# Kernel tuning notes

Measured on AMD Instinct MI355X. Metric: run time of the kernel, lower is better.

Reference implementation:

```python
import jax, jax.numpy as jnp
import numpy as np

NEG = 9e15

def adj_helper(adj):
    n = adj.shape[0]
    a = adj + jnp.eye(n, dtype=adj.dtype)
    d1 = jnp.sqrt(a.sum(axis=-1))[:, None]
    d2 = jnp.sqrt(a.sum(axis=0))[None, :]
    return a / d1 / d2

def gcn(adj, x, Ws):
    a = adj_helper(adj)
    z = x
    for W in Ws:
        z = jax.nn.elu(a @ (z @ W))
    return z

def sage(adj, x, layers):
    deg = jnp.clip(adj.sum(axis=-1, keepdims=True), 1e-5, None)
    a = adj / deg
    z = x
    for (Wp, b, W) in layers:
        h = jax.nn.elu(z @ Wp + b)
        h = a @ h
        z = jax.nn.elu(jnp.concatenate([z, h], axis=1) @ W)
    return z

def sim_graph_cos(h, k):
    n = h.shape[0]
    length = jnp.sqrt(jnp.sum(h * h, axis=-1))          # [n]
    sim = (h @ h.T) / (length[:, None] * length[None, :])
    sim = sim - jnp.eye(n, dtype=sim.dtype) * NEG        # mask self
    val, ids = jax.lax.top_k(sim, k)                     # [n,k]
    rows = jnp.arange(n)[:, None]
    return jnp.zeros_like(sim).at[rows, ids].set(val)

def setup_inputs() -> dict:
    key = jax.random.key(0)
    ks = jax.random.split(key, 16)
    N, F, H, E, K = 6144, 128, 128, 16384, 32
    s = 0.05
    adj = (jax.random.uniform(ks[0], (N, N)) < 0.002).astype(jnp.float32)
    x = jax.random.normal(ks[1], (N, F), dtype=jnp.float32)
    src = jax.random.randint(ks[2], (E,), 0, N)
    dst = jax.random.randint(ks[3], (E,), 0, N)
    labels = (jax.random.uniform(ks[4], (E,)) < 0.5).astype(jnp.float32)
    return {
        "src": src, "dst": dst, "labels": labels, "adj": adj, "x": x,
        "Wg1": jax.random.normal(ks[5], (F, H)) * s,
        "Wg2": jax.random.normal(ks[6], (H, H)) * s,
        "Wp1": jax.random.normal(ks[7], (F, H)) * s,
        "b1": jax.random.normal(ks[8], (1, H)) * s,
        "Ws1": jax.random.normal(ks[9], (F + H, H)) * s,
        "Wp2": jax.random.normal(ks[10], (H, H)) * s,
        "b2": jax.random.normal(ks[11], (1, H)) * s,
        "Ws2": jax.random.normal(ks[12], (H + H, H)) * s,
        "PredW": jax.random.normal(ks[13], (2 * H, 2 * H)) * s,
        "PredB": jax.random.normal(ks[14], (1, 1)) * s,
        "top_k": 32,
    }

def reference(src, dst, labels, adj, x, Wg1, Wg2, Wp1, b1, Ws1, Wp2, b2, Ws2, PredW, PredB, top_k):
    h1 = gcn(adj, x, [Wg1, Wg2])                 # [N,H]
    sim_adj = sim_graph_cos(x, top_k)            # [N,N] top-k sparse (dense-stored)
    h2 = sage(sim_adj, x, [(Wp1, b1, Ws1), (Wp2, b2, Ws2)])  # [N,H]
    h = jnp.concatenate([h1, h2], axis=1)        # [N,2H]
    src_h = h[src]                               # [E,2H]
    dst_h = h[dst]                               # [E,2H]
    logits = jnp.einsum('ed,df,ef->e', src_h, PredW, dst_h) + PredB[0, 0]
    # BCEWithLogitsLoss (mean, numerically stable)
    loss = jnp.mean(jnp.maximum(logits, 0) - logits * labels
                    + jnp.log1p(jnp.exp(-jnp.abs(logits))))
    return loss, logits
```

## Files before the change

kernel.cpp:

```cpp
#include <hip/hip_runtime.h>
#include <hip/hip_bf16.h>
#include <stdint.h>

#define N_NODES 6144
#define FDIM    128
#define EEDGES  16384
#define KTOP    32
#define KSEL    48
#define MAXNBR  64
#define MAXCAND 512
#define NTILES  96
#define GRIDY   16
#define TPB     (NTILES/GRIDY)

typedef short bf16x8 __attribute__((ext_vector_type(8)));
typedef float f32x4  __attribute__((ext_vector_type(4)));

__device__ __forceinline__ float elu_f(float x){ return x > 0.f ? x : expm1f(x); }

__device__ __forceinline__ unsigned short f2bf(float f){
  unsigned int u = __float_as_uint(f);
  u += 0x7FFFu + ((u >> 16) & 1u);
  return (unsigned short)(u >> 16);
}
__device__ __forceinline__ float bf2f(unsigned short h){
  return __uint_as_float(((unsigned int)h) << 16);
}

__global__ __launch_bounds__(256) void prep(const float* __restrict__ adj,
    const float* __restrict__ x, int* __restrict__ nbr, int* __restrict__ nbrcnt,
    int* __restrict__ colcnt, unsigned short* __restrict__ xbf,
    float* __restrict__ xninv, float* __restrict__ cat1){
  const int b = blockIdx.x, t = threadIdx.x;
  if (b < N_NODES){
    const int i = b;
    __shared__ int s_cnt;
    if (t == 0) s_cnt = 0;
    __syncthreads();
    const float4* row = (const float4*)(adj + (size_t)i * N_NODES);
    for (int v = t; v < N_NODES/4; v += 256){
      float4 f = row[v];
      int c = v * 4;
      if (f.x != 0.f){ int s = atomicAdd(&s_cnt,1); if (s < MAXNBR) nbr[i*MAXNBR+s] = c;   atomicAdd(&colcnt[c],1); }
      if (f.y != 0.f){ int s = atomicAdd(&s_cnt,1); if (s < MAXNBR) nbr[i*MAXNBR+s] = c+1; atomicAdd(&colcnt[c+1],1); }
      if (f.z != 0.f){ int s = atomicAdd(&s_cnt,1); if (s < MAXNBR) nbr[i*MAXNBR+s] = c+2; atomicAdd(&colcnt[c+2],1); }
      if (f.w != 0.f){ int s = atomicAdd(&s_cnt,1); if (s < MAXNBR) nbr[i*MAXNBR+s] = c+3; atomicAdd(&colcnt[c+3],1); }
    }
    __syncthreads();
    if (t == 0) nbrcnt[i] = min(s_cnt, MAXNBR);
  } else {
    const int i = (b - N_NODES)*2 + (t >> 7);
    const int tl = t & 127;
    float v = x[(size_t)i*FDIM + tl];
    xbf[(size_t)i*FDIM + tl] = f2bf(v);
    cat1[(size_t)i*256 + tl] = v;
    float s = v * v;
    for (int o = 32; o > 0; o >>= 1) s += __shfl_down(s, o, 64);
    __shared__ float ws[4];
    if ((t & 63) == 0) ws[t >> 6] = s;
    __syncthreads();
    if (tl == 0) xninv[i] = rsqrtf(ws[(t>>7)*2] + ws[(t>>7)*2 + 1]);
  }
}

__global__ __launch_bounds__(256) void simgemm(const unsigned short* __restrict__ xbf,
    const float* __restrict__ xninv, unsigned short* __restrict__ sim,
    float* __restrict__ gmax){
  const int t    = threadIdx.x;
  const int R0   = blockIdx.x * 32;
  const int tb0  = blockIdx.y * TPB;
  const int lane = t & 63, w = t >> 6;
  const int lr   = lane & 15, q8 = (lane >> 4) * 8, quad = lane >> 4;

  __shared__ unsigned short Abf[32][136];
  __shared__ unsigned short Bbf[64][136];
  __shared__ unsigned short Stile[32][72];
  __shared__ float nrow[32];
  __shared__ float ncol[64];
  __shared__ float wmax[4][32];

  for (int e = t; e < 32*16; e += 256){
    int r = e >> 4, c8 = e & 15;
    *(uint4*)&Abf[r][c8*8] = ((const uint4*)(xbf + (size_t)(R0 + r)*FDIM))[c8];
  }
  if (t < 32) nrow[t] = xninv[R0 + t];

  for (int tb = tb0; tb < tb0 + TPB; ++tb){
    __syncthreads();
    for (int e = t; e < 64*16; e += 256){
      int r = e >> 4, c8 = e & 15;
      *(uint4*)&Bbf[r][c8*8] = ((const uint4*)(xbf + (size_t)(tb*64 + r)*FDIM))[c8];
    }
    if (t < 64) ncol[t] = xninv[tb*64 + t];
    __syncthreads();

    f32x4 acc[2] = {};
#pragma unroll
    for (int kb = 0; kb < 4; ++kb){
      bf16x8 bcol  = *(const bf16x8*)&Bbf[w*16 + lr][kb*32 + q8];
      bf16x8 arow0 = *(const bf16x8*)&Abf[lr      ][kb*32 + q8];
      bf16x8 arow1 = *(const bf16x8*)&Abf[16 + lr ][kb*32 + q8];
      acc[0] = __builtin_amdgcn_mfma_f32_16x16x32_bf16(bcol, arow0, acc[0], 0, 0, 0);
      acc[1] = __builtin_amdgcn_mfma_f32_16x16x32_bf16(bcol, arow1, acc[1], 0, 0, 0);
    }
    const int scol0 = w*16 + quad*4;
    const float nc0 = ncol[scol0], nc1 = ncol[scol0+1],
                nc2 = ncol[scol0+2], nc3 = ncol[scol0+3];
#pragma unroll
    for (int f = 0; f < 2; ++f){
      const int srow = f*16 + lr;
      const float nr = nrow[srow];
      const int grow = R0 + srow, gcol0 = tb*64 + scol0;
      float v0 = acc[f][0]*nr*nc0, v1 = acc[f][1]*nr*nc1,
            v2 = acc[f][2]*nr*nc2, v3 = acc[f][3]*nr*nc3;
      if (grow == gcol0    ) v0 = -2.0f;
      if (grow == gcol0 + 1) v1 = -2.0f;
      if (grow == gcol0 + 2) v2 = -2.0f;
      if (grow == gcol0 + 3) v3 = -2.0f;
      unsigned int h0 = f2bf(v0), h1 = f2bf(v1), h2 = f2bf(v2), h3 = f2bf(v3);
      uint2 p; p.x = h0 | (h1 << 16); p.y = h2 | (h3 << 16);
      *(uint2*)&Stile[srow][scol0] = p;
      float rmax = fmaxf(fmaxf(bf2f(h0), bf2f(h1)), fmaxf(bf2f(h2), bf2f(h3)));
      rmax = fmaxf(rmax, __shfl_xor(rmax, 16, 64));
      rmax = fmaxf(rmax, __shfl_xor(rmax, 32, 64));
      if (quad == 0) wmax[w][srow] = rmax;
    }
    __syncthreads();
    {
      int r = t >> 3, c8 = t & 7;
      *(uint4*)&sim[(size_t)(R0 + r)*N_NODES + tb*64 + c8*8] = *(uint4*)&Stile[r][c8*8];
    }
    if (t < 32){
      float g = fmaxf(fmaxf(wmax[0][t], wmax[1][t]), fmaxf(wmax[2][t], wmax[3][t]));
      gmax[(size_t)(R0 + t)*NTILES + tb] = g;
    }
  }
}

__global__ __launch_bounds__(256) void refine_scan(const float* __restrict__ x,
    const float* __restrict__ xninv, const unsigned short* __restrict__ sim,
    const float* __restrict__ gmax, float* __restrict__ tval, int* __restrict__ tidx,
    float* __restrict__ deginv){
  const int i = blockIdx.x, t = threadIdx.x;
  __shared__ float xi[128];
  __shared__ float gm[NTILES];
  __shared__ float tauv;
  __shared__ float cv[MAXCAND];
  __shared__ int   ci[MAXCAND];
  __shared__ float sel[KTOP];
  __shared__ int   cnt;
  if (t == 0) cnt = 0;
  if (t < 32) *(float4*)&xi[t*4] = *(const float4*)(x + (size_t)i*FDIM + t*4);
  if (t < NTILES) gm[t] = gmax[(size_t)i*NTILES + t];
  __syncthreads();
  if (t < NTILES){
    float v = gm[t]; int rank = 0;
    for (int j = 0; j < NTILES; ++j){
      float u = gm[j];
      if (u > v || (u == v && j < t)) rank++;
    }
    if (rank == KSEL-1) tauv = v;
  }
  __syncthreads();
  const float taui = tauv;
  const uint4* srow = (const uint4*)(sim + (size_t)i*N_NODES);
  for (int v8 = t; v8 < N_NODES/8; v8 += 256){
    uint4 u = srow[v8];
    const unsigned short* h = (const unsigned short*)&u;
#pragma unroll
    for (int q = 0; q < 8; ++q){
      if (bf2f(h[q]) >= taui){
        int s = atomicAdd(&cnt, 1);
        if (s < MAXCAND) ci[s] = v8*8 + q;
      }
    }
  }
  __syncthreads();
  int n = cnt; if (n > MAXCAND) n = MAXCAND;
  const float ni = xninv[i];
  const int part = t & 3, cb = t >> 2;
  for (int c0 = 0; c0 < n; c0 += 64){
    const int c = c0 + cb;
    float acc = 0.f;
    int idx = 0;
    if (c < n){
      idx = ci[c];
      const float* xc = x + (size_t)idx*FDIM + part*32;
#pragma unroll
      for (int q = 0; q < 8; ++q){
        float4 f = *(const float4*)(xc + q*4);
        const float* a = &xi[part*32 + q*4];
        acc += a[0]*f.x + a[1]*f.y + a[2]*f.z + a[3]*f.w;
      }
    }
    acc += __shfl_xor(acc, 1, 64);
    acc += __shfl_xor(acc, 2, 64);
    if (c < n && part == 0) cv[c] = acc * ni * xninv[idx];
  }
  __syncthreads();
  for (int c = t; c < n; c += 256){
    float v = cv[c]; int id = ci[c];
    int rank = 0;
    for (int j = 0; j < n; ++j){
      float u = cv[j];
      if (u > v || (u == v && ci[j] < id)) rank++;
    }
    if (rank < KTOP){
      tval[(size_t)i*KTOP + rank] = v;
      tidx[(size_t)i*KTOP + rank] = id;
      sel[rank] = v;
    }
  }
  __syncthreads();
  if (t == 0){
    float s = 0.f;
    for (int q = 0; q < KTOP; ++q) s += sel[q];
    deginv[i] = 1.0f / fmaxf(s, 1e-5f);
  }
}

__global__ __launch_bounds__(256) void gemm_dual(const float* __restrict__ A,
    const float* __restrict__ B1, const float* __restrict__ B2,
    const float* __restrict__ bias2, float* __restrict__ C1, float* __restrict__ C2,
    const int* __restrict__ nbrcnt, const int* __restrict__ colcnt,
    float* __restrict__ d1inv, float* __restrict__ d2inv){
  const int t = threadIdx.x;
  const int R0 = blockIdx.x * 32, C0 = blockIdx.y * 64;
  if (blockIdx.y == 0 && t < 32){
    int i = R0 + t;
    d1inv[i] = rsqrtf((float)(nbrcnt[i] + 1));
    d2inv[i] = rsqrtf((float)(colcnt[i] + 1));
  }
  const int rg = t >> 4, cg = t & 15;
  __shared__ float Alds[32][34];
  __shared__ float B1lds[32][68];
  __shared__ float B2lds[32][68];
  float4 p0 = {0,0,0,0}, p1 = {0,0,0,0};
  float4 q0 = {0,0,0,0}, q1 = {0,0,0,0};
  for (int kc = 0; kc < FDIM; kc += 32){
    __syncthreads();
    { int r = t >> 3, k0 = (t & 7) * 4;
      float4 f = *(const float4*)(A + (size_t)(R0 + r)*FDIM + kc + k0);
      Alds[k0+0][r] = f.x; Alds[k0+1][r] = f.y; Alds[k0+2][r] = f.z; Alds[k0+3][r] = f.w; }
#pragma unroll
    for (int e = 0; e < 2; ++e){
      int idx = t + e*256;
      int k = idx >> 4, m4 = idx & 15;
      *(float4*)&B1lds[k][m4*4] = *(const float4*)(B1 + (size_t)(kc + k)*FDIM + C0 + m4*4);
      *(float4*)&B2lds[k][m4*4] = *(const float4*)(B2 + (size_t)(kc + k)*FDIM + C0 + m4*4);
    }
    __syncthreads();
#pragma unroll
    for (int k = 0; k < 32; ++k){
      float2 a = *(const float2*)&Alds[k][rg*2];
      float4 b = *(const float4*)&B1lds[k][cg*4];
      float4 c = *(const float4*)&B2lds[k][cg*4];
      p0.x += a.x*b.x; p0.y += a.x*b.y; p0.z += a.x*b.z; p0.w += a.x*b.w;
      p1.x += a.y*b.x; p1.y += a.y*b.y; p1.z += a.y*b.z; p1.w += a.y*b.w;
      q0.x += a.x*c.x; q0.y += a.x*c.y; q0.z += a.x*c.z; q0.w += a.x*c.w;
      q1.x += a.y*c.x; q1.y += a.y*c.y; q1.z += a.y*c.z; q1.w += a.y*c.w;
    }
  }
  const int r0 = R0 + rg*2, c0 = C0 + cg*4;
  *(float4*)&C1[(size_t)r0*FDIM + c0] = p0;
  *(float4*)&C1[(size_t)(r0+1)*FDIM + c0] = p1;
  float4 bb = *(const float4*)&bias2[c0];
  q0.x = elu_f(q0.x + bb.x); q0.y = elu_f(q0.y + bb.y); q0.z = elu_f(q0.z + bb.z); q0.w = elu_f(q0.w + bb.w);
  q1.x = elu_f(q1.x + bb.x); q1.y = elu_f(q1.y + bb.y); q1.z = elu_f(q1.z + bb.z); q1.w = elu_f(q1.w + bb.w);
  *(float4*)&C2[(size_t)r0*FDIM + c0] = q0;
  *(float4*)&C2[(size_t)(r0+1)*FDIM + c0] = q1;
}

template<int M>
__global__ __launch_bounds__(256) void gemm_k(const float* __restrict__ A, int lda,
    const float* __restrict__ B, const float* __restrict__ bias,
    float* __restrict__ C, int ldc, int K, int act){
  const int t = threadIdx.x;
  const int R0 = blockIdx.x * 32, C0 = blockIdx.y * 64;
  const int rg = t >> 4, cg = t & 15;
  __shared__ float Alds[32][34];
  __shared__ float Blds[32][68];
  float4 acc0 = {0,0,0,0}, acc1 = {0,0,0,0};
  for (int kc = 0; kc < K; kc += 32){
    __syncthreads();
    { int r = t >> 3, k0 = (t & 7) * 4;
      float4 f = *(const float4*)(A + (size_t)(R0 + r)*lda + kc + k0);
      Alds[k0+0][r] = f.x; Alds[k0+1][r] = f.y; Alds[k0+2][r] = f.z; Alds[k0+3][r] = f.w; }
#pragma unroll
    for (int e = 0; e < 2; ++e){
      int idx = t + e*256;
      int k = idx >> 4, m4 = idx & 15;
      *(float4*)&Blds[k][m4*4] = *(const float4*)(B + (size_t)(kc + k)*M + C0 + m4*4);
    }
    __syncthreads();
#pragma unroll
    for (int k = 0; k < 32; ++k){
      float2 a = *(const float2*)&Alds[k][rg*2];
      float4 b = *(const float4*)&Blds[k][cg*4];
      acc0.x += a.x*b.x; acc0.y += a.x*b.y; acc0.z += a.x*b.z; acc0.w += a.x*b.w;
      acc1.x += a.y*b.x; acc1.y += a.y*b.y; acc1.z += a.y*b.z; acc1.w += a.y*b.w;
    }
  }
  const int r0 = R0 + rg*2, c0 = C0 + cg*4;
  float4 bb = {0,0,0,0};
  if (bias) bb = *(const float4*)&bias[c0];
  acc0.x += bb.x; acc0.y += bb.y; acc0.z += bb.z; acc0.w += bb.w;
  acc1.x += bb.x; acc1.y += bb.y; acc1.z += bb.z; acc1.w += bb.w;
  if (act){
    acc0.x = elu_f(acc0.x); acc0.y = elu_f(acc0.y); acc0.z = elu_f(acc0.z); acc0.w = elu_f(acc0.w);
    acc1.x = elu_f(acc1.x); acc1.y = elu_f(acc1.y); acc1.z = elu_f(acc1.z); acc1.w = elu_f(acc1.w);
  }
  *(float4*)&C[(size_t)r0*ldc + c0] = acc0;
  *(float4*)&C[(size_t)(r0+1)*ldc + c0] = acc1;
}

__global__ __launch_bounds__(128) void spmm_gcn(const float* __restrict__ T,
    const int* __restrict__ nbr, const int* __restrict__ nbrcnt,
    const float* __restrict__ d1inv, const float* __restrict__ d2inv,
    float* __restrict__ C, int ldc){
  const int i = blockIdx.x, t = threadIdx.x;
  float acc = T[(size_t)i*FDIM + t] * d2inv[i];
  const int cnt = nbrcnt[i];
  const int* nb = nbr + (size_t)i*MAXNBR;
  for (int s = 0; s < cnt; ++s){
    int j = nb[s];
    acc += T[(size_t)j*FDIM + t] * d2inv[j];
  }
  C[(size_t)i*ldc + t] = elu_f(acc * d1inv[i]);
}

__global__ __launch_bounds__(128) void spmm_sage(const float* __restrict__ P,
    const float* __restrict__ tval, const int* __restrict__ tidx,
    const float* __restrict__ deginv, float* __restrict__ C, int ldc){
  const int i = blockIdx.x, t = threadIdx.x;
  float acc = 0.f;
  const float* vv = tval + (size_t)i*KTOP;
  const int*   ii = tidx + (size_t)i*KTOP;
  for (int s = 0; s < KTOP; ++s)
    acc += vv[s] * P[(size_t)ii[s]*FDIM + t];
  C[(size_t)i*ldc + t] = acc * deginv[i];
}

__global__ __launch_bounds__(128) void spmm_pair(const float* __restrict__ T1,
    const int* __restrict__ nbr, const int* __restrict__ nbrcnt,
    const float* __restrict__ d1inv, const float* __restrict__ d2inv,
    float* __restrict__ z1,
    const float* __restrict__ T2, const float* __restrict__ tval,
    const int* __restrict__ tidx, const float* __restrict__ deginv,
    float* __restrict__ cat1r){
  const int b = blockIdx.x, t = threadIdx.x;
  if (b < N_NODES){
    const int i = b;
    float acc = T1[(size_t)i*FDIM + t] * d2inv[i];
    const int cnt = nbrcnt[i];
    const int* nb = nbr + (size_t)i*MAXNBR;
    for (int s = 0; s < cnt; ++s){
      int j = nb[s];
      acc += T1[(size_t)j*FDIM + t] * d2inv[j];
    }
    z1[(size_t)i*FDIM + t] = elu_f(acc * d1inv[i]);
  } else {
    const int i = b - N_NODES;
    float acc = 0.f;
    const float* vv = tval + (size_t)i*KTOP;
    const int*   ii = tidx + (size_t)i*KTOP;
    for (int s = 0; s < KTOP; ++s)
      acc += vv[s] * T2[(size_t)ii[s]*FDIM + t];
    cat1r[(size_t)i*256 + t] = acc * deginv[i];
  }
}

__global__ __launch_bounds__(256) void edge_loss(const int* __restrict__ src,
    const int* __restrict__ dst, const float* __restrict__ labels,
    const float* __restrict__ HP, const float* __restrict__ hcat,
    const float* __restrict__ predB, float* __restrict__ out,
    float* __restrict__ partial){
  const int t = threadIdx.x;
  const int e = blockIdx.x*4 + (t >> 6);
  const int lane = t & 63;
  const int s = src[e], d = dst[e];
  const float* hp = HP   + (size_t)s*256;
  const float* hc = hcat + (size_t)d*256;
  float acc = 0.f;
  for (int k = lane; k < 256; k += 64) acc += hp[k] * hc[k];
  for (int o = 32; o > 0; o >>= 1) acc += __shfl_down(acc, o, 64);
  __shared__ float terms[4];
  if (lane == 0){
    float l = acc + predB[0];
    out[1 + e] = l;
    float y = labels[e];
    terms[t >> 6] = fmaxf(l, 0.f) - l*y + log1pf(expf(-fabsf(l)));
  }
  __syncthreads();
  if (t == 0) partial[blockIdx.x] = terms[0] + terms[1] + terms[2] + terms[3];
}

__global__ __launch_bounds__(256) void reduce_loss(const float* __restrict__ partial,
    float* __restrict__ out){
  const int t = threadIdx.x, lane = t & 63, w = t >> 6;
  float s = 0.f;
  for (int i = t; i < EEDGES/4; i += 256) s += partial[i];
  for (int o = 32; o > 0; o >>= 1) s += __shfl_down(s, o, 64);
  __shared__ float ws[4];
  if (lane == 0) ws[w] = s;
  __syncthreads();
  if (t == 0) out[0] = (ws[0] + ws[1] + ws[2] + ws[3]) * (1.0f / EEDGES);
}

extern "C" void kernel_launch(void* const* d_in, const int* in_sizes, int n_in,
                              void* d_out, int out_size, void* d_ws, size_t ws_size,
                              hipStream_t stream){
  (void)in_sizes; (void)n_in; (void)out_size; (void)ws_size;
  const int*   src    = (const int*)d_in[0];
  const int*   dst    = (const int*)d_in[1];
  const float* labels = (const float*)d_in[2];
  const float* adj    = (const float*)d_in[3];
  const float* x      = (const float*)d_in[4];
  const float* Wg1    = (const float*)d_in[5];
  const float* Wg2    = (const float*)d_in[6];
  const float* Wp1    = (const float*)d_in[7];
  const float* b1     = (const float*)d_in[8];
  const float* Ws1    = (const float*)d_in[9];
  const float* Wp2    = (const float*)d_in[10];
  const float* b2     = (const float*)d_in[11];
  const float* Ws2    = (const float*)d_in[12];
  const float* PredW  = (const float*)d_in[13];
  const float* PredB  = (const float*)d_in[14];

  char* ws = (char*)d_ws;
  size_t off = 0;
  auto alloc = [&](size_t bytes)->void*{
    void* p = ws + off; off += (bytes + 255) & ~(size_t)255; return p; };

  int*   colcnt = (int*)  alloc((size_t)N_NODES*4);
  int*   nbrcnt = (int*)  alloc((size_t)N_NODES*4);
  int*   nbr    = (int*)  alloc((size_t)N_NODES*MAXNBR*4);
  float* d1inv  = (float*)alloc((size_t)N_NODES*4);
  float* d2inv  = (float*)alloc((size_t)N_NODES*4);
  float* xninv  = (float*)alloc((size_t)N_NODES*4);
  unsigned short* xbf = (unsigned short*)alloc((size_t)N_NODES*FDIM*2);
  float* tval   = (float*)alloc((size_t)N_NODES*KTOP*4);
  int*   tidx   = (int*)  alloc((size_t)N_NODES*KTOP*4);
  float* dginv  = (float*)alloc((size_t)N_NODES*4);
  float* gmax   = (float*)alloc((size_t)N_NODES*NTILES*4);
  float* partial= (float*)alloc((size_t)(EEDGES/4)*4);
  float* T1     = (float*)alloc((size_t)N_NODES*FDIM*4);
  float* T2     = (float*)alloc((size_t)N_NODES*FDIM*4);
  float* cat1   = (float*)alloc((size_t)N_NODES*256*4);
  float* cat2   = (float*)alloc((size_t)N_NODES*256*4);
  float* hcat   = (float*)alloc((size_t)N_NODES*256*4);
  unsigned short* sim = (unsigned short*)alloc((size_t)N_NODES*N_NODES*2);
  float* z1     = cat2;
  float* out    = (float*)d_out;

  hipMemsetAsync(colcnt, 0, (size_t)N_NODES*4, stream);

  prep       <<<N_NODES + N_NODES/2, 256, 0, stream>>>(adj, x, nbr, nbrcnt, colcnt, xbf, xninv, cat1);
  simgemm    <<<dim3(N_NODES/32, GRIDY), 256, 0, stream>>>(xbf, xninv, sim, gmax);
  refine_scan<<<N_NODES, 256, 0, stream>>>(x, xninv, sim, gmax, tval, tidx, dginv);

  gemm_dual  <<<dim3(N_NODES/32, 2), 256, 0, stream>>>(x, Wg1, Wp1, b1, T1, T2,
                                                       nbrcnt, colcnt, d1inv, d2inv);
  spmm_pair  <<<2*N_NODES, 128, 0, stream>>>(T1, nbr, nbrcnt, d1inv, d2inv, z1,
                                             T2, tval, tidx, dginv, cat1 + 128);

  gemm_k<128><<<dim3(N_NODES/32, 2), 256, 0, stream>>>(z1, FDIM, Wg2, nullptr, T1, FDIM, 128, 0);
  spmm_gcn   <<<N_NODES, 128, 0, stream>>>(T1, nbr, nbrcnt, d1inv, d2inv, hcat, 256);

  gemm_k<128><<<dim3(N_NODES/32, 2), 256, 0, stream>>>(cat1, 256, Ws1, nullptr, cat2, 256, 256, 1);

  gemm_k<128><<<dim3(N_NODES/32, 2), 256, 0, stream>>>(cat2, 256, Wp2, b2, T1, FDIM, 128, 1);
  spmm_sage  <<<N_NODES, 128, 0, stream>>>(T1, tval, tidx, dginv, cat2 + 128, 256);
  gemm_k<128><<<dim3(N_NODES/32, 2), 256, 0, stream>>>(cat2, 256, Ws2, nullptr, hcat + 128, 256, 256, 1);

  gemm_k<256><<<dim3(N_NODES/32, 4), 256, 0, stream>>>(hcat, 256, PredW, nullptr, cat1, 256, 256, 0);
  edge_loss  <<<EEDGES/4, 256, 0, stream>>>(src, dst, labels, cat1, hcat, PredB, out, partial);
  reduce_loss<<<1, 256, 0, stream>>>(partial, out);
}
```

Baseline: 483.8 us.

## Merge independent GCN and SAGE stages into shared launches; enlarge simgemm row tile

Independent GEMMs from the GCN and SAGE branches (Wg2 and Ws1) now run in one launch, and the GCN spmm runs alongside the Wp2 GEMM in a second, with blocks split by index. This cuts kernel launches and lets small, under-filled grids overlap on the GPU. z1 gets its own buffer so it no longer aliases cat2. The similarity GEMM now tiles 64 rows per block instead of 32, reusing each B-tile load across four MFMAs per wave, at the cost of more LDS and a grid half as large.

```diff
diff --git a/kernel.cpp b/kernel.cpp
--- a/kernel.cpp
+++ b/kernel.cpp
@@ -67,23 +67,23 @@
     const float* __restrict__ xninv, unsigned short* __restrict__ sim,
     float* __restrict__ gmax){
   const int t    = threadIdx.x;
-  const int R0   = blockIdx.x * 32;
+  const int R0   = blockIdx.x * 64;
   const int tb0  = blockIdx.y * TPB;
   const int lane = t & 63, w = t >> 6;
   const int lr   = lane & 15, q8 = (lane >> 4) * 8, quad = lane >> 4;
 
-  __shared__ unsigned short Abf[32][136];
+  __shared__ unsigned short Abf[64][136];
   __shared__ unsigned short Bbf[64][136];
-  __shared__ unsigned short Stile[32][72];
-  __shared__ float nrow[32];
+  __shared__ unsigned short Stile[64][72];
+  __shared__ float nrow[64];
   __shared__ float ncol[64];
-  __shared__ float wmax[4][32];
-
-  for (int e = t; e < 32*16; e += 256){
+  __shared__ float wmax[4][64];
+
+  for (int e = t; e < 64*16; e += 256){
     int r = e >> 4, c8 = e & 15;
     *(uint4*)&Abf[r][c8*8] = ((const uint4*)(xbf + (size_t)(R0 + r)*FDIM))[c8];
   }
-  if (t < 32) nrow[t] = xninv[R0 + t];
+  if (t < 64) nrow[t] = xninv[R0 + t];
 
   for (int tb = tb0; tb < tb0 + TPB; ++tb){
     __syncthreads();
@@ -94,20 +94,21 @@
     if (t < 64) ncol[t] = xninv[tb*64 + t];
     __syncthreads();
 
-    f32x4 acc[2] = {};
+    f32x4 acc[4] = {};
 #pragma unroll
     for (int kb = 0; kb < 4; ++kb){
-      bf16x8 bcol  = *(const bf16x8*)&Bbf[w*16 + lr][kb*32 + q8];
-      bf16x8 arow0 = *(const bf16x8*)&Abf[lr      ][kb*32 + q8];
-      bf16x8 arow1 = *(const bf16x8*)&Abf[16 + lr ][kb*32 + q8];
-      acc[0] = __builtin_amdgcn_mfma_f32_16x16x32_bf16(bcol, arow0, acc[0], 0, 0, 0);
-      acc[1] = __builtin_amdgcn_mfma_f32_16x16x32_bf16(bcol, arow1, acc[1], 0, 0, 0);
+      bf16x8 bcol = *(const bf16x8*)&Bbf[w*16 + lr][kb*32 + q8];
+#pragma unroll
+      for (int f = 0; f < 4; ++f){
+        bf16x8 arow = *(const bf16x8*)&Abf[f*16 + lr][kb*32 + q8];
+        acc[f] = __builtin_amdgcn_mfma_f32_16x16x32_bf16(bcol, arow, acc[f], 0, 0, 0);
+      }
     }
     const int scol0 = w*16 + quad*4;
     const float nc0 = ncol[scol0], nc1 = ncol[scol0+1],
                 nc2 = ncol[scol0+2], nc3 = ncol[scol0+3];
 #pragma unroll
-    for (int f = 0; f < 2; ++f){
+    for (int f = 0; f < 4; ++f){
       const int srow = f*16 + lr;
       const float nr = nrow[srow];
       const int grow = R0 + srow, gcol0 = tb*64 + scol0;
@@ -126,11 +127,13 @@
       if (quad == 0) wmax[w][srow] = rmax;
     }
     __syncthreads();
-    {
-      int r = t >> 3, c8 = t & 7;
+#pragma unroll
+    for (int e0 = 0; e0 < 2; ++e0){
+      int e = t + e0*256;
+      int r = e >> 3, c8 = e & 7;
       *(uint4*)&sim[(size_t)(R0 + r)*N_NODES + tb*64 + c8*8] = *(uint4*)&Stile[r][c8*8];
     }
-    if (t < 32){
+    if (t < 64){
       float g = fmaxf(fmaxf(wmax[0][t], wmax[1][t]), fmaxf(wmax[2][t], wmax[3][t]));
       gmax[(size_t)(R0 + t)*NTILES + tb] = g;
     }
@@ -219,6 +222,47 @@
   }
 }
 
+__device__ __forceinline__ void gemm_body(const float* __restrict__ A, int lda,
+    const float* __restrict__ B, int ldb, const float* __restrict__ bias,
+    float* __restrict__ C, int ldc, int K, int act, int R0, int C0){
+  const int t = threadIdx.x;
+  const int rg = t >> 4, cg = t & 15;
+  __shared__ float Alds[32][34];
+  __shared__ float Blds[32][68];
+  float4 acc0 = {0,0,0,0}, acc1 = {0,0,0,0};
+  for (int kc = 0; kc < K; kc += 32){
+    __syncthreads();
+    { int r = t >> 3, k0 = (t & 7) * 4;
+      float4 f = *(const float4*)(A + (size_t)(R0 + r)*lda + kc + k0);
+      Alds[k0+0][r] = f.x; Alds[k0+1][r] = f.y; Alds[k0+2][r] = f.z; Alds[k0+3][r] = f.w; }
+#pragma unroll
+    for (int e = 0; e < 2; ++e){
+      int idx = t + e*256;
+      int k = idx >> 4, m4 = idx & 15;
+      *(float4*)&Blds[k][m4*4] = *(const float4*)(B + (size_t)(kc + k)*ldb + C0 + m4*4);
+    }
+    __syncthreads();
+#pragma unroll
+    for (int k = 0; k < 32; ++k){
+      float2 a = *(const float2*)&Alds[k][rg*2];
+      float4 b = *(const float4*)&Blds[k][cg*4];
+      acc0.x += a.x*b.x; acc0.y += a.x*b.y; acc0.z += a.x*b.z; acc0.w += a.x*b.w;
+      acc1.x += a.y*b.x; acc1.y += a.y*b.y; acc1.z += a.y*b.z; acc1.w += a.y*b.w;
+    }
+  }
+  const int r0 = R0 + rg*2, c0 = C0 + cg*4;
+  float4 bb = {0,0,0,0};
+  if (bias) bb = *(const float4*)&bias[c0];
+  acc0.x += bb.x; acc0.y += bb.y; acc0.z += bb.z; acc0.w += bb.w;
+  acc1.x += bb.x; acc1.y += bb.y; acc1.z += bb.z; acc1.w += bb.w;
+  if (act){
+    acc0.x = elu_f(acc0.x); acc0.y = elu_f(acc0.y); acc0.z = elu_f(acc0.z); acc0.w = elu_f(acc0.w);
+    acc1.x = elu_f(acc1.x); acc1.y = elu_f(acc1.y); acc1.z = elu_f(acc1.z); acc1.w = elu_f(acc1.w);
+  }
+  *(float4*)&C[(size_t)r0*ldc + c0] = acc0;
+  *(float4*)&C[(size_t)(r0+1)*ldc + c0] = acc1;
+}
+
 __global__ __launch_bounds__(256) void gemm_dual(const float* __restrict__ A,
     const float* __restrict__ B1, const float* __restrict__ B2,
     const float* __restrict__ bias2, float* __restrict__ C1, float* __restrict__ C2,
@@ -275,70 +319,7 @@
 __global__ __launch_bounds__(256) void gemm_k(const float* __restrict__ A, int lda,
     const float* __restrict__ B, const float* __restrict__ bias,
     float* __restrict__ C, int ldc, int K, int act){
-  const int t = threadIdx.x;
-  const int R0 = blockIdx.x * 32, C0 = blockIdx.y * 64;
-  const int rg = t >> 4, cg = t & 15;
-  __shared__ float Alds[32][34];
-  __shared__ float Blds[32][68];
-  float4 acc0 = {0,0,0,0}, acc1 = {0,0,0,0};
-  for (int kc = 0; kc < K; kc += 32){
-    __syncthreads();
-    { int r = t >> 3, k0 = (t & 7) * 4;
-      float4 f = *(const float4*)(A + (size_t)(R0 + r)*lda + kc + k0);
-      Alds[k0+0][r] = f.x; Alds[k0+1][r] = f.y; Alds[k0+2][r] = f.z; Alds[k0+3][r] = f.w; }
-#pragma unroll
-    for (int e = 0; e < 2; ++e){
-      int idx = t + e*256;
-      int k = idx >> 4, m4 = idx & 15;
-      *(float4*)&Blds[k][m4*4] = *(const float4*)(B + (size_t)(kc + k)*M + C0 + m4*4);
-    }
-    __syncthreads();
-#pragma unroll
-    for (int k = 0; k < 32; ++k){
-      float2 a = *(const float2*)&Alds[k][rg*2];
-      float4 b = *(const float4*)&Blds[k][cg*4];
-      acc0.x += a.x*b.x; acc0.y += a.x*b.y; acc0.z += a.x*b.z; acc0.w += a.x*b.w;
-      acc1.x += a.y*b.x; acc1.y += a.y*b.y; acc1.z += a.y*b.z; acc1.w += a.y*b.w;
-    }
-  }
-  const int r0 = R0 + rg*2, c0 = C0 + cg*4;
-  float4 bb = {0,0,0,0};
-  if (bias) bb = *(const float4*)&bias[c0];
-  acc0.x += bb.x; acc0.y += bb.y; acc0.z += bb.z; acc0.w += bb.w;
-  acc1.x += bb.x; acc1.y += bb.y; acc1.z += bb.z; acc1.w += bb.w;
-  if (act){
-    acc0.x = elu_f(acc0.x); acc0.y = elu_f(acc0.y); acc0.z = elu_f(acc0.z); acc0.w = elu_f(acc0.w);
-    acc1.x = elu_f(acc1.x); acc1.y = elu_f(acc1.y); acc1.z = elu_f(acc1.z); acc1.w = elu_f(acc1.w);
-  }
-  *(float4*)&C[(size_t)r0*ldc + c0] = acc0;
-  *(float4*)&C[(size_t)(r0+1)*ldc + c0] = acc1;
-}
-
-__global__ __launch_bounds__(128) void spmm_gcn(const float* __restrict__ T,
-    const int* __restrict__ nbr, const int* __restrict__ nbrcnt,
-    const float* __restrict__ d1inv, const float* __restrict__ d2inv,
-    float* __restrict__ C, int ldc){
-  const int i = blockIdx.x, t = threadIdx.x;
-  float acc = T[(size_t)i*FDIM + t] * d2inv[i];
-  const int cnt = nbrcnt[i];
-  const int* nb = nbr + (size_t)i*MAXNBR;
-  for (int s = 0; s < cnt; ++s){
-    int j = nb[s];
-    acc += T[(size_t)j*FDIM + t] * d2inv[j];
-  }
-  C[(size_t)i*ldc + t] = elu_f(acc * d1inv[i]);
-}
-
-__global__ __launch_bounds__(128) void spmm_sage(const float* __restrict__ P,
-    const float* __restrict__ tval, const int* __restrict__ tidx,
-    const float* __restrict__ deginv, float* __restrict__ C, int ldc){
-  const int i = blockIdx.x, t = threadIdx.x;
-  float acc = 0.f;
-  const float* vv = tval + (size_t)i*KTOP;
-  const int*   ii = tidx + (size_t)i*KTOP;
-  for (int s = 0; s < KTOP; ++s)
-    acc += vv[s] * P[(size_t)ii[s]*FDIM + t];
-  C[(size_t)i*ldc + t] = acc * deginv[i];
+  gemm_body(A, lda, B, M, bias, C, ldc, K, act, blockIdx.x*32, blockIdx.y*64);
 }
 
 __global__ __launch_bounds__(128) void spmm_pair(const float* __restrict__ T1,
@@ -368,6 +349,58 @@
       acc += vv[s] * T2[(size_t)ii[s]*FDIM + t];
     cat1r[(size_t)i*256 + t] = acc * deginv[i];
   }
+}
+
+__global__ __launch_bounds__(256) void dual_stage1(const float* __restrict__ z1,
+    const float* __restrict__ Wg2, float* __restrict__ T1,
+    const float* __restrict__ cat1, const float* __restrict__ Ws1,
+    float* __restrict__ cat2){
+  const int b = blockIdx.x;
+  if (b < 384){
+    gemm_body(z1, FDIM, Wg2, FDIM, nullptr, T1, FDIM, FDIM, 0,
+              (b % 192)*32, (b / 192)*64);
+  } else {
+    const int bb = b - 384;
+    gemm_body(cat1, 256, Ws1, FDIM, nullptr, cat2, 256, 256, 1,
+              (bb % 192)*32, (bb / 192)*64);
+  }
+}
+
+__global__ __launch_bounds__(256) void dual_stage2(const float* __restrict__ T1,
+    const int* __restrict__ nbr, const int* __restrict__ nbrcnt,
+    const float* __restrict__ d1inv, const float* __restrict__ d2inv,
+    float* __restrict__ hcat,
+    const float* __restrict__ cat2, const float* __restrict__ Wp2,
+    const float* __restrict__ b2, float* __restrict__ T2){
+  const int b = blockIdx.x, t = threadIdx.x;
+  if (b < 3072){
+    const int i = b*2 + (t >> 7);
+    const int tl = t & 127;
+    float acc = T1[(size_t)i*FDIM + tl] * d2inv[i];
+    const int cnt = nbrcnt[i];
+    const int* nb = nbr + (size_t)i*MAXNBR;
+    for (int s = 0; s < cnt; ++s){
+      int j = nb[s];
+      acc += T1[(size_t)j*FDIM + tl] * d2inv[j];
+    }
+    hcat[(size_t)i*256 + tl] = elu_f(acc * d1inv[i]);
+  } else {
+    const int bb = b - 3072;
+    gemm_body(cat2, 256, Wp2, FDIM, b2, T2, FDIM, FDIM, 1,
+              (bb % 192)*32, (bb / 192)*64);
+  }
+}
+
+__global__ __launch_bounds__(128) void spmm_sage(const float* __restrict__ P,
+    const float* __restrict__ tval, const int* __restrict__ tidx,
+    const float* __restrict__ deginv, float* __restrict__ C, int ldc){
+  const int i = blockIdx.x, t = threadIdx.x;
+  float acc = 0.f;
+  const float* vv = tval + (size_t)i*KTOP;
+  const int*   ii = tidx + (size_t)i*KTOP;
+  for (int s = 0; s < KTOP; ++s)
+    acc += vv[s] * P[(size_t)ii[s]*FDIM + t];
+  C[(size_t)i*ldc + t] = acc * deginv[i];
 }
 
 __global__ __launch_bounds__(256) void edge_loss(const int* __restrict__ src,
@@ -446,31 +479,27 @@
   float* partial= (float*)alloc((size_t)(EEDGES/4)*4);
   float* T1     = (float*)alloc((size_t)N_NODES*FDIM*4);
   float* T2     = (float*)alloc((size_t)N_NODES*FDIM*4);
+  float* z1     = (float*)alloc((size_t)N_NODES*FDIM*4);
   float* cat1   = (float*)alloc((size_t)N_NODES*256*4);
   float* cat2   = (float*)alloc((size_t)N_NODES*256*4);
   float* hcat   = (float*)alloc((size_t)N_NODES*256*4);
   unsigned short* sim = (unsigned short*)alloc((size_t)N_NODES*N_NODES*2);
-  float* z1     = cat2;
   float* out    = (float*)d_out;
 
   hipMemsetAsync(colcnt, 0, (size_t)N_NODES*4, stream);
 
   prep       <<<N_NODES + N_NODES/2, 256, 0, stream>>>(adj, x, nbr, nbrcnt, colcnt, xbf, xninv, cat1);
-  simgemm    <<<dim3(N_NODES/32, GRIDY), 256, 0, stream>>>(xbf, xninv, sim, gmax);
+  simgemm    <<<dim3(N_NODES/64, GRIDY), 256, 0, stream>>>(xbf, xninv, sim, gmax);
   refine_scan<<<N_NODES, 256, 0, stream>>>(x, xninv, sim, gmax, tval, tidx, dginv);
 
   gemm_dual  <<<dim3(N_NODES/32, 2), 256, 0, stream>>>(x, Wg1, Wp1, b1, T1, T2,
                                                        nbrcnt, colcnt, d1inv, d2inv);
   spmm_pair  <<<2*N_NODES, 128, 0, stream>>>(T1, nbr, nbrcnt, d1inv, d2inv, z1,
                                              T2, tval, tidx, dginv, cat1 + 128);
-
-  gemm_k<128><<<dim3(N_NODES/32, 2), 256, 0, stream>>>(z1, FDIM, Wg2, nullptr, T1, FDIM, 128, 0);
-  spmm_gcn   <<<N_NODES, 128, 0, stream>>>(T1, nbr, nbrcnt, d1inv, d2inv, hcat, 256);
-
-  gemm_k<128><<<dim3(N_NODES/32, 2), 256, 0, stream>>>(cat1, 256, Ws1, nullptr, cat2, 256, 256, 1);
-
-  gemm_k<128><<<dim3(N_NODES/32, 2), 256, 0, stream>>>(cat2, 256, Wp2, b2, T1, FDIM, 128, 1);
-  spmm_sage  <<<N_NODES, 128, 0, stream>>>(T1, tval, tidx, dginv, cat2 + 128, 256);
+  dual_stage1<<<768, 256, 0, stream>>>(z1, Wg2, T1, cat1, Ws1, cat2);
+  dual_stage2<<<3072 + 384, 256, 0, stream>>>(T1, nbr, nbrcnt, d1inv, d2inv, hcat,
+                                              cat2, Wp2, b2, T2);
+  spmm_sage  <<<N_NODES, 128, 0, stream>>>(T2, tval, tidx, dginv, cat2 + 128, 256);
   gemm_k<128><<<dim3(N_NODES/32, 2), 256, 0, stream>>>(cat2, 256, Ws2, nullptr, hcat + 128, 256, 256, 1);
 
   gemm_k<256><<<dim3(N_NODES/32, 4), 256, 0, stream>>>(hcat, 256, PredW, nullptr, cat1, 256, 256, 0);
```

Measured after the change: 471.2 us. -2.6%, faster.
